# Performance work log

Hardware: AMD Instinct MI355X
Metric: run time of the kernel (lower is better)

## Reference

```python
import jax, jax.numpy as jnp
import numpy as np

F_DIM = 128
NUM_RES = 2

def setup_inputs() -> dict:
    key = jax.random.key(0)
    ks = jax.random.split(key, 12)
    N, B, F = 500000, 4096, F_DIM
    s = 1.0 / np.sqrt(F)
    inp = {
        "x": jax.random.normal(ks[0], (N, F), dtype=jnp.float32),
        "E": jax.random.normal(ks[1], (B,), dtype=jnp.float32),
        "num_batch": B,
        "batch_seg": jnp.sort(jax.random.randint(ks[2], (N,), 0, B).astype(jnp.int64)),
        # linear_q: Dense(F, F)
        "Wq": jax.random.normal(ks[3], (F, F), dtype=jnp.float32) * s,
        "bq": jnp.zeros((F,), dtype=jnp.float32),
        # linear_k: Dense(1, F, bias=True)
        "Wk": jax.random.normal(ks[4], (1, F), dtype=jnp.float32),
        "bk": jnp.zeros((F,), dtype=jnp.float32),
        # residual block: 2 dense layers of size F
        "W1": jax.random.normal(ks[5], (F, F), dtype=jnp.float32) * s,
        "b1": jnp.zeros((F,), dtype=jnp.float32),
        "W2": jax.random.normal(ks[6], (F, F), dtype=jnp.float32) * s,
        "b2": jnp.zeros((F,), dtype=jnp.float32),
    }
    return inp

def reference(x, E, num_batch, batch_seg, Wq, bq, Wk, bk, W1, b1, W2, b2):
    F = x.shape[1]
    # q = linear_q(x): [N, F]
    q = x @ Wq + bq
    # e = |E|[:, None] -> linear_k: [num_batch, F], gathered to atoms [N, F]
    e = jnp.abs(E)[:, None]
    k = (e @ Wk + bk)[batch_seg]
    embed = jax.nn.softplus(k * q)                       # [N, F]
    embed_total = jnp.sum(embed, axis=1)                 # [N]
    # per-molecule segment sums and atom counts
    pred_embed = jax.ops.segment_sum(embed_total, batch_seg, num_segments=num_batch)
    per_natom = jax.ops.segment_sum(jnp.ones_like(embed_total), batch_seg, num_segments=num_batch)
    # broadcast correction back to atoms
    d_embed = ((E - pred_embed) / per_natom)[batch_seg]  # [N]
    scale_embed = embed + d_embed[:, None] / F
    # residual block: x + dense2(silu(dense1(silu(x))))
    h = scale_embed
    h = jax.nn.silu(h) @ W1 + b1
    h = jax.nn.silu(h) @ W2 + b2
    return scale_embed + h
```

## Files before the change

### kernel.cpp

```cpp
#include <hip/hip_runtime.h>
#include <cstdint>

#define F_DIM 128
#define XSTR 136

typedef short s16x8 __attribute__((ext_vector_type(8)));
typedef float f32x4 __attribute__((ext_vector_type(4)));

__device__ __forceinline__ uint32_t f2bf(float f){
    uint32_t u = __float_as_uint(f);
    return (u + 0x7FFFu + ((u >> 16) & 1u)) >> 16;
}
__device__ __forceinline__ uint32_t packbf2(float lo, float hi){
    return f2bf(lo) | (f2bf(hi) << 16);
}
__device__ __forceinline__ uint2 cvt4(float4 v){
    return make_uint2(packbf2(v.x, v.y), packbf2(v.z, v.w));
}
__device__ __forceinline__ float softplus_f(float v){
    return fmaxf(v, 0.f) + __logf(1.f + __expf(-fabsf(v)));
}
__device__ __forceinline__ float silu_f(float v){
    return __fdividef(v, 1.f + __expf(-v));
}
__device__ __forceinline__ float rowsum16(float p){
    p += __int_as_float(__builtin_amdgcn_update_dpp(0, __float_as_int(p), 0x121, 0xF, 0xF, false));
    p += __int_as_float(__builtin_amdgcn_update_dpp(0, __float_as_int(p), 0x122, 0xF, 0xF, false));
    p += __int_as_float(__builtin_amdgcn_update_dpp(0, __float_as_int(p), 0x124, 0xF, 0xF, false));
    p += __int_as_float(__builtin_amdgcn_update_dpp(0, __float_as_int(p), 0x128, 0xF, 0xF, false));
    return p;
}

__global__ void k_prep(float* __restrict__ zeroed, int B){
    int gid = blockIdx.x*blockDim.x + threadIdx.x;
    if (gid < 2*B) zeroed[gid] = 0.f;
}

__global__ void __launch_bounds__(512, 8) k_embed(
    const float* __restrict__ x, const int* __restrict__ seg,
    const float* __restrict__ Wq, const float* __restrict__ bq,
    const float* __restrict__ E, const float* __restrict__ Wk,
    const float* __restrict__ bk, float* __restrict__ out,
    float* __restrict__ pred, float* __restrict__ natom, int N)
{
    __shared__ __align__(16) short xs[128*XSTR];
    __shared__ __align__(16) float rs[128];
    __shared__ __align__(16) float es[128];
    __shared__ int ss[128];
    const int tid  = threadIdx.x;
    const int wave = tid >> 6, lane = tid & 63;
    const int quad = lane >> 4, ln = lane & 15;
    const int mycol = wave*16 + ln;

    s16x8 wf[4];
    #pragma unroll
    for (int s = 0; s < 4; ++s)
        #pragma unroll
        for (int j = 0; j < 8; ++j)
            wf[s][j] = (short)f2bf(Wq[(size_t)(s*32 + quad*8 + j)*F_DIM + mycol]);
    const float biasv = bq[mycol];
    const float wkv = Wk[mycol];
    const float bkv = bk[mycol];

    const int lrow = tid >> 5, lc4 = tid & 31;
    const int nt = (N + 127) >> 7;
    for (int tile = blockIdx.x; tile < nt; tile += gridDim.x){
        const int base = tile << 7;
        if (tid < 128){
            int r = base + tid;
            int sg = (r < N) ? seg[r] : 0;
            ss[tid] = sg;
            es[tid] = fabsf(E[sg]);
            rs[tid] = 0.f;
        }
        {
            const float4* xp = (const float4*)x + (size_t)(base + lrow)*32 + lc4;
            short* xsp = &xs[lrow*XSTR + lc4*4];
            #pragma unroll
            for (int j = 0; j < 8; ++j){
                if (base + lrow + j*16 < N)
                    *(uint2*)xsp = cvt4(*xp);
                xp  += 16*32;
                xsp += 16*XSTR;
            }
        }
        __syncthreads();

        float* orow = out + (size_t)(base + quad*4)*F_DIM + mycol;
        const short* arow = &xs[ln*XSTR + quad*8];
        #pragma unroll
        for (int rt = 0; rt < 8; ++rt){
            f32x4 acc = {0.f, 0.f, 0.f, 0.f};
            #pragma unroll
            for (int s = 0; s < 4; ++s){
                s16x8 a = *(const s16x8*)(arow + rt*16*XSTR + s*32);
                acc = __builtin_amdgcn_mfma_f32_16x16x32_bf16(a, wf[s], acc, 0, 0, 0);
            }
            const int row0 = rt*16 + quad*4;
            f32x4 e4 = *(const f32x4*)&es[row0];
            #pragma unroll
            for (int reg = 0; reg < 4; ++reg){
                if (base + row0 + reg < N){
                    float kv = e4[reg]*wkv + bkv;
                    float e = softplus_f(kv * (acc[reg] + biasv));
                    orow[rt*16*F_DIM + reg*F_DIM] = e;
                    float p = rowsum16(e);
                    if (ln == 0) atomicAdd(&rs[row0 + reg], p);
                }
            }
        }
        __syncthreads();
        if (tid < 128 && base + tid < N){
            atomicAdd(&pred[ss[tid]], rs[tid]);
            atomicAdd(&natom[ss[tid]], 1.f);
        }
        __syncthreads();
    }
}

__global__ void k_dsc(const float* __restrict__ E, const float* __restrict__ pred,
                      const float* __restrict__ natom, float* __restrict__ dsc, int B){
    int b = blockIdx.x*blockDim.x + threadIdx.x;
    if (b < B) dsc[b] = (E[b] - pred[b]) / natom[b] * (1.0f/128.0f);
}

__global__ void __launch_bounds__(512, 6) k_resid(
    const int* __restrict__ seg, const float* __restrict__ dsc,
    const float* __restrict__ W1, const float* __restrict__ b1,
    const float* __restrict__ W2, const float* __restrict__ b2,
    float* __restrict__ out, int N)
{
    __shared__ __align__(16) short xs[128*XSTR];
    __shared__ __align__(16) float dsl[128];
    const int tid  = threadIdx.x;
    const int wave = tid >> 6, lane = tid & 63;
    const int quad = lane >> 4, ln = lane & 15;
    const int mycol = wave*16 + ln;

    s16x8 w1f[4], w2f[4];
    #pragma unroll
    for (int s = 0; s < 4; ++s)
        #pragma unroll
        for (int j = 0; j < 8; ++j){
            int k = s*32 + quad*8 + j;
            w1f[s][j] = (short)f2bf(W1[(size_t)k*F_DIM + mycol]);
            w2f[s][j] = (short)f2bf(W2[(size_t)k*F_DIM + mycol]);
        }
    const float b1v = b1[mycol], b2v = b2[mycol];

    const int lrow = tid >> 5, lc4 = tid & 31;
    const int nt = (N + 127) >> 7;
    for (int tile = blockIdx.x; tile < nt; tile += gridDim.x){
        const int base = tile << 7;
        {
            const float4* op = (const float4*)out + (size_t)(base + lrow)*32 + lc4;
            short* xsp = &xs[lrow*XSTR + lc4*4];
            #pragma unroll
            for (int j = 0; j < 8; ++j){
                int r = base + lrow + j*16;
                if (r < N){
                    float dv = dsc[seg[r]];
                    if (lc4 == 0) dsl[lrow + j*16] = dv;
                    float4 v = *op;
                    float4 t;
                    t.x = silu_f(v.x + dv); t.y = silu_f(v.y + dv);
                    t.z = silu_f(v.z + dv); t.w = silu_f(v.w + dv);
                    *(uint2*)xsp = cvt4(t);
                }
                op  += 16*32;
                xsp += 16*XSTR;
            }
        }
        __syncthreads();

        uint32_t hp[16];
        const short* arow = &xs[ln*XSTR + quad*8];
        #pragma unroll
        for (int rt = 0; rt < 8; ++rt){
            f32x4 acc = {0.f, 0.f, 0.f, 0.f};
            #pragma unroll
            for (int s = 0; s < 4; ++s){
                s16x8 a = *(const s16x8*)(arow + rt*16*XSTR + s*32);
                acc = __builtin_amdgcn_mfma_f32_16x16x32_bf16(a, w1f[s], acc, 0, 0, 0);
            }
            hp[rt*2]   = packbf2(silu_f(acc[0]+b1v), silu_f(acc[1]+b1v));
            hp[rt*2+1] = packbf2(silu_f(acc[2]+b1v), silu_f(acc[3]+b1v));
        }
        __syncthreads();

        {
            short* tp = &xs[(quad*4)*XSTR + mycol];
            #pragma unroll
            for (int rt = 0; rt < 8; ++rt){
                tp[(rt*16+0)*XSTR] = (short)(hp[rt*2]   & 0xFFFFu);
                tp[(rt*16+1)*XSTR] = (short)(hp[rt*2]   >> 16);
                tp[(rt*16+2)*XSTR] = (short)(hp[rt*2+1] & 0xFFFFu);
                tp[(rt*16+3)*XSTR] = (short)(hp[rt*2+1] >> 16);
            }
        }
        __syncthreads();

        float* orow = out + (size_t)(base + quad*4)*F_DIM + mycol;
        #pragma unroll
        for (int rt = 0; rt < 8; ++rt){
            f32x4 acc = {0.f, 0.f, 0.f, 0.f};
            #pragma unroll
            for (int s = 0; s < 4; ++s){
                s16x8 a = *(const s16x8*)(arow + rt*16*XSTR + s*32);
                acc = __builtin_amdgcn_mfma_f32_16x16x32_bf16(a, w2f[s], acc, 0, 0, 0);
            }
            const int row0 = rt*16 + quad*4;
            f32x4 d4 = *(const f32x4*)&dsl[row0];
            #pragma unroll
            for (int reg = 0; reg < 4; ++reg){
                if (base + row0 + reg < N){
                    float se = orow[rt*16*F_DIM + reg*F_DIM] + d4[reg];
                    orow[rt*16*F_DIM + reg*F_DIM] = se + acc[reg] + b2v;
                }
            }
        }
        __syncthreads();
    }
}

extern "C" void kernel_launch(void* const* d_in, const int* in_sizes, int n_in,
                              void* d_out, int out_size, void* d_ws, size_t ws_size,
                              hipStream_t stream)
{
    const float* x  = (const float*)d_in[0];
    const float* E  = (const float*)d_in[1];
    const int*  seg = (const int*)d_in[3];
    const float* Wq = (const float*)d_in[4];
    const float* bq = (const float*)d_in[5];
    const float* Wk = (const float*)d_in[6];
    const float* bk = (const float*)d_in[7];
    const float* W1 = (const float*)d_in[8];
    const float* b1 = (const float*)d_in[9];
    const float* W2 = (const float*)d_in[10];
    const float* b2 = (const float*)d_in[11];
    float* out = (float*)d_out;
    int N = in_sizes[0] / F_DIM;
    int B = in_sizes[1];

    float* pred  = (float*)d_ws;
    float* natom = pred + B;
    float* dsc   = natom + B;

    hipLaunchKernelGGL(k_prep, dim3((2*B + 255)/256), dim3(256), 0, stream,
                       pred, B);
    hipLaunchKernelGGL(k_embed, dim3(1024), dim3(512), 0, stream,
                       x, seg, Wq, bq, E, Wk, bk, out, pred, natom, N);
    hipLaunchKernelGGL(k_dsc, dim3((B + 255)/256), dim3(256), 0, stream,
                       E, pred, natom, dsc, B);
    hipLaunchKernelGGL(k_resid, dim3(768), dim3(512), 0, stream,
                       seg, dsc, W1, b1, W2, b2, out, N);
}
```

Before: 854.5 us.

## Recompute embedding in residual kernel instead of storing and reloading it

The first pass now only computes per-molecule sums and no longer writes the embed tensor to out. A new fused kernel reloads x, recomputes the Q projection and softplus, adds the correction, and runs both residual dense layers, writing out once. This removes one full write and one full read of the N×F intermediate, at the cost of a redundant GEMM plus transcendentals. It also raises register pressure from three weight fragment sets and a per-thread se buffer. Full-tile fast paths drop the per-row bounds checks.

```diff
diff --git a/kernel.cpp b/kernel.cpp
--- a/kernel.cpp
+++ b/kernel.cpp
@@ -36,11 +36,11 @@
     if (gid < 2*B) zeroed[gid] = 0.f;
 }
 
-__global__ void __launch_bounds__(512, 8) k_embed(
+__global__ void __launch_bounds__(512, 8) k_sum(
     const float* __restrict__ x, const int* __restrict__ seg,
     const float* __restrict__ Wq, const float* __restrict__ bq,
     const float* __restrict__ E, const float* __restrict__ Wk,
-    const float* __restrict__ bk, float* __restrict__ out,
+    const float* __restrict__ bk,
     float* __restrict__ pred, float* __restrict__ natom, int N)
 {
     __shared__ __align__(16) short xs[128*XSTR];
@@ -66,6 +66,7 @@
     const int nt = (N + 127) >> 7;
     for (int tile = blockIdx.x; tile < nt; tile += gridDim.x){
         const int base = tile << 7;
+        const bool full = (base + 128 <= N);
         if (tid < 128){
             int r = base + tid;
             int sg = (r < N) ? seg[r] : 0;
@@ -76,17 +77,27 @@
         {
             const float4* xp = (const float4*)x + (size_t)(base + lrow)*32 + lc4;
             short* xsp = &xs[lrow*XSTR + lc4*4];
-            #pragma unroll
-            for (int j = 0; j < 8; ++j){
-                if (base + lrow + j*16 < N)
-                    *(uint2*)xsp = cvt4(*xp);
-                xp  += 16*32;
-                xsp += 16*XSTR;
-            }
-        }
-        __syncthreads();
-
-        float* orow = out + (size_t)(base + quad*4)*F_DIM + mycol;
+            if (full){
+                float4 v0 = xp[0*512], v1 = xp[1*512], v2 = xp[2*512], v3 = xp[3*512];
+                float4 v4 = xp[4*512], v5 = xp[5*512], v6 = xp[6*512], v7 = xp[7*512];
+                *(uint2*)&xsp[0*16*XSTR] = cvt4(v0);
+                *(uint2*)&xsp[1*16*XSTR] = cvt4(v1);
+                *(uint2*)&xsp[2*16*XSTR] = cvt4(v2);
+                *(uint2*)&xsp[3*16*XSTR] = cvt4(v3);
+                *(uint2*)&xsp[4*16*XSTR] = cvt4(v4);
+                *(uint2*)&xsp[5*16*XSTR] = cvt4(v5);
+                *(uint2*)&xsp[6*16*XSTR] = cvt4(v6);
+                *(uint2*)&xsp[7*16*XSTR] = cvt4(v7);
+            } else {
+                #pragma unroll
+                for (int j = 0; j < 8; ++j){
+                    if (base + lrow + j*16 < N) *(uint2*)&xsp[j*16*XSTR] = cvt4(xp[j*512]);
+                    else                        *(uint2*)&xsp[j*16*XSTR] = make_uint2(0u, 0u);
+                }
+            }
+        }
+        __syncthreads();
+
         const short* arow = &xs[ln*XSTR + quad*8];
         #pragma unroll
         for (int rt = 0; rt < 8; ++rt){
@@ -100,10 +111,9 @@
             f32x4 e4 = *(const f32x4*)&es[row0];
             #pragma unroll
             for (int reg = 0; reg < 4; ++reg){
-                if (base + row0 + reg < N){
+                if (full || base + row0 + reg < N){
                     float kv = e4[reg]*wkv + bkv;
                     float e = softplus_f(kv * (acc[reg] + biasv));
-                    orow[rt*16*F_DIM + reg*F_DIM] = e;
                     float p = rowsum16(e);
                     if (ln == 0) atomicAdd(&rs[row0 + reg], p);
                 }
@@ -124,57 +134,106 @@
     if (b < B) dsc[b] = (E[b] - pred[b]) / natom[b] * (1.0f/128.0f);
 }
 
-__global__ void __launch_bounds__(512, 6) k_resid(
-    const int* __restrict__ seg, const float* __restrict__ dsc,
+__global__ void __launch_bounds__(512, 4) k_main(
+    const float* __restrict__ x, const int* __restrict__ seg,
+    const float* __restrict__ Wq, const float* __restrict__ bq,
+    const float* __restrict__ E, const float* __restrict__ Wk,
+    const float* __restrict__ bk, const float* __restrict__ dsc,
     const float* __restrict__ W1, const float* __restrict__ b1,
     const float* __restrict__ W2, const float* __restrict__ b2,
     float* __restrict__ out, int N)
 {
     __shared__ __align__(16) short xs[128*XSTR];
+    __shared__ __align__(16) float es[128];
     __shared__ __align__(16) float dsl[128];
     const int tid  = threadIdx.x;
     const int wave = tid >> 6, lane = tid & 63;
     const int quad = lane >> 4, ln = lane & 15;
     const int mycol = wave*16 + ln;
 
-    s16x8 w1f[4], w2f[4];
+    s16x8 wqf[4], w1f[4], w2f[4];
     #pragma unroll
     for (int s = 0; s < 4; ++s)
         #pragma unroll
         for (int j = 0; j < 8; ++j){
             int k = s*32 + quad*8 + j;
+            wqf[s][j] = (short)f2bf(Wq[(size_t)k*F_DIM + mycol]);
             w1f[s][j] = (short)f2bf(W1[(size_t)k*F_DIM + mycol]);
             w2f[s][j] = (short)f2bf(W2[(size_t)k*F_DIM + mycol]);
         }
+    const float biasv = bq[mycol];
+    const float wkv = Wk[mycol];
+    const float bkv = bk[mycol];
     const float b1v = b1[mycol], b2v = b2[mycol];
 
     const int lrow = tid >> 5, lc4 = tid & 31;
     const int nt = (N + 127) >> 7;
     for (int tile = blockIdx.x; tile < nt; tile += gridDim.x){
         const int base = tile << 7;
+        const bool full = (base + 128 <= N);
+        if (tid < 128){
+            int r = base + tid;
+            int sg = (r < N) ? seg[r] : 0;
+            es[tid]  = fabsf(E[sg]);
+            dsl[tid] = dsc[sg];
+        }
         {
-            const float4* op = (const float4*)out + (size_t)(base + lrow)*32 + lc4;
+            const float4* xp = (const float4*)x + (size_t)(base + lrow)*32 + lc4;
             short* xsp = &xs[lrow*XSTR + lc4*4];
-            #pragma unroll
-            for (int j = 0; j < 8; ++j){
-                int r = base + lrow + j*16;
-                if (r < N){
-                    float dv = dsc[seg[r]];
-                    if (lc4 == 0) dsl[lrow + j*16] = dv;
-                    float4 v = *op;
-                    float4 t;
-                    t.x = silu_f(v.x + dv); t.y = silu_f(v.y + dv);
-                    t.z = silu_f(v.z + dv); t.w = silu_f(v.w + dv);
-                    *(uint2*)xsp = cvt4(t);
+            if (full){
+                float4 v0 = xp[0*512], v1 = xp[1*512], v2 = xp[2*512], v3 = xp[3*512];
+                float4 v4 = xp[4*512], v5 = xp[5*512], v6 = xp[6*512], v7 = xp[7*512];
+                *(uint2*)&xsp[0*16*XSTR] = cvt4(v0);
+                *(uint2*)&xsp[1*16*XSTR] = cvt4(v1);
+                *(uint2*)&xsp[2*16*XSTR] = cvt4(v2);
+                *(uint2*)&xsp[3*16*XSTR] = cvt4(v3);
+                *(uint2*)&xsp[4*16*XSTR] = cvt4(v4);
+                *(uint2*)&xsp[5*16*XSTR] = cvt4(v5);
+                *(uint2*)&xsp[6*16*XSTR] = cvt4(v6);
+                *(uint2*)&xsp[7*16*XSTR] = cvt4(v7);
+            } else {
+                #pragma unroll
+                for (int j = 0; j < 8; ++j){
+                    if (base + lrow + j*16 < N) *(uint2*)&xsp[j*16*XSTR] = cvt4(xp[j*512]);
+                    else                        *(uint2*)&xsp[j*16*XSTR] = make_uint2(0u, 0u);
                 }
-                op  += 16*32;
-                xsp += 16*XSTR;
-            }
+            }
+        }
+        __syncthreads();
+
+        float se[32];
+        const short* arow = &xs[ln*XSTR + quad*8];
+        #pragma unroll
+        for (int rt = 0; rt < 8; ++rt){
+            f32x4 acc = {0.f, 0.f, 0.f, 0.f};
+            #pragma unroll
+            for (int s = 0; s < 4; ++s){
+                s16x8 a = *(const s16x8*)(arow + rt*16*XSTR + s*32);
+                acc = __builtin_amdgcn_mfma_f32_16x16x32_bf16(a, wqf[s], acc, 0, 0, 0);
+            }
+            const int row0 = rt*16 + quad*4;
+            f32x4 e4 = *(const f32x4*)&es[row0];
+            f32x4 d4 = *(const f32x4*)&dsl[row0];
+            #pragma unroll
+            for (int reg = 0; reg < 4; ++reg){
+                float kv = e4[reg]*wkv + bkv;
+                float e = softplus_f(kv * (acc[reg] + biasv));
+                se[rt*4 + reg] = e + d4[reg];
+            }
+        }
+        __syncthreads();
+
+        {
+            short* tp = &xs[(quad*4)*XSTR + mycol];
+            #pragma unroll
+            for (int rt = 0; rt < 8; ++rt)
+                #pragma unroll
+                for (int r = 0; r < 4; ++r)
+                    tp[(rt*16 + r)*XSTR] = (short)f2bf(silu_f(se[rt*4 + r]));
         }
         __syncthreads();
 
         uint32_t hp[16];
-        const short* arow = &xs[ln*XSTR + quad*8];
         #pragma unroll
         for (int rt = 0; rt < 8; ++rt){
             f32x4 acc = {0.f, 0.f, 0.f, 0.f};
@@ -210,13 +269,10 @@
                 acc = __builtin_amdgcn_mfma_f32_16x16x32_bf16(a, w2f[s], acc, 0, 0, 0);
             }
             const int row0 = rt*16 + quad*4;
-            f32x4 d4 = *(const f32x4*)&dsl[row0];
             #pragma unroll
             for (int reg = 0; reg < 4; ++reg){
-                if (base + row0 + reg < N){
-                    float se = orow[rt*16*F_DIM + reg*F_DIM] + d4[reg];
-                    orow[rt*16*F_DIM + reg*F_DIM] = se + acc[reg] + b2v;
-                }
+                if (full || base + row0 + reg < N)
+                    orow[rt*16*F_DIM + reg*F_DIM] = se[rt*4+reg] + acc[reg] + b2v;
             }
         }
         __syncthreads();
@@ -248,10 +304,10 @@
 
     hipLaunchKernelGGL(k_prep, dim3((2*B + 255)/256), dim3(256), 0, stream,
                        pred, B);
-    hipLaunchKernelGGL(k_embed, dim3(1024), dim3(512), 0, stream,
-                       x, seg, Wq, bq, E, Wk, bk, out, pred, natom, N);
+    hipLaunchKernelGGL(k_sum, dim3(1024), dim3(512), 0, stream,
+                       x, seg, Wq, bq, E, Wk, bk, pred, natom, N);
     hipLaunchKernelGGL(k_dsc, dim3((B + 255)/256), dim3(256), 0, stream,
                        E, pred, natom, dsc, B);
-    hipLaunchKernelGGL(k_resid, dim3(768), dim3(512), 0, stream,
-                       seg, dsc, W1, b1, W2, b2, out, N);
-}
+    hipLaunchKernelGGL(k_main, dim3(512), dim3(512), 0, stream,
+                       x, seg, Wq, bq, E, Wk, bk, dsc, W1, b1, W2, b2, out, N);
+}
```

Measured after the change: 738.2 us. 13.6% less time.
